# Performance work log

Measured on AMD Instinct MI355X. Metric: run time of the kernel, lower is better.

Reference implementation:

```python
import jax, jax.numpy as jnp
import numpy as np

N_NODES = 50000
N_EDGES = 800000
D_IN = 512
D_OUT = 128

def setup_inputs() -> dict:
    key = jax.random.key(0)
    k1, k2, k3, k4, k5, k6 = jax.random.split(key, 6)
    std = 1.0 / np.sqrt(D_OUT)
    x = jax.random.normal(k1, (N_NODES, D_IN), dtype=jnp.float32)
    edge_w = jax.random.uniform(k2, (N_EDGES,), dtype=jnp.float32)
    src = jax.random.randint(k3, (N_EDGES,), 0, N_NODES, dtype=jnp.int32)
    dst = jax.random.randint(k4, (N_EDGES,), 0, N_NODES, dtype=jnp.int32)
    W = jax.random.uniform(k5, (D_IN, D_OUT), minval=-std, maxval=std, dtype=jnp.float32)
    b = jax.random.uniform(k6, (D_OUT,), minval=-std, maxval=std, dtype=jnp.float32)
    return {"x": x, "edge_w": edge_w, "src": src, "dst": dst, "W": W, "b": b}

def reference(x, edge_w, src, dst, W, b):
    # Dense GEMM: [N, D_in] @ [D_in, D_out]
    h = x @ W
    # SpMM with COO adjacency: out[i] = sum_{e: dst[e]==i} edge_w[e] * h[src[e]]
    msg = h[src] * edge_w[:, None]          # [E, D_out]
    agg = jax.ops.segment_sum(msg, dst, num_segments=N_NODES)
    return agg + b
```

## Files before the change

kernel.cpp:

```cpp
#include <hip/hip_runtime.h>
#include <hip/hip_bf16.h>

#define M_NODES  50000
#define D_IN_K   512
#define D_OUT_N  128
#define N_EDGES  800000
#define SCAN_NBLK 49
#define PAD 16

typedef short  bf16x8 __attribute__((ext_vector_type(8)));
typedef float  f32x4  __attribute__((ext_vector_type(4)));

static __device__ __forceinline__ unsigned short f2bf(float f) {
    unsigned u = __float_as_uint(f);
    unsigned r = u + 0x7FFF + ((u >> 16) & 1);
    return (unsigned short)(r >> 16);
}
static __device__ __forceinline__ float bflo(unsigned q) { return __uint_as_float(q << 16); }
static __device__ __forceinline__ float bfhi(unsigned q) { return __uint_as_float(q & 0xFFFF0000u); }

__global__ __launch_bounds__(256) void permw_kernel(const float* __restrict__ W,
                                                    unsigned short* __restrict__ Wp) {
    int tid = blockIdx.x * 256 + threadIdx.x;
    int lane = tid & 63;
    int nt   = (tid >> 6) & 7;
    int kb4  = tid >> 9;
    int n    = nt * 16 + (lane & 15);
    int kbase = kb4 * 32 + ((lane >> 4) & 3) * 8;
    unsigned short frag[8];
#pragma unroll
    for (int j = 0; j < 8; ++j)
        frag[j] = f2bf(W[(size_t)(kbase + j) * D_OUT_N + n]);
    *(uint4*)&Wp[(size_t)tid * 8] = *(const uint4*)frag;
}

__global__ __launch_bounds__(256, 2) void mfma_gemm_hist_kernel(const float* __restrict__ x,
                                                                const uint4* __restrict__ Wp4,
                                                                unsigned short* __restrict__ h,
                                                                const int* __restrict__ dst,
                                                                int* __restrict__ counts) {
    __shared__ uint4 wlds[4096];

    const int wave = threadIdx.x >> 6;
    const int lane = threadIdx.x & 63;
    const int m0   = blockIdx.x * 128 + wave * 32;
    const int mrow = lane & 15;
    const int kgrp = lane >> 4;

    const int r0 = m0 + mrow;
    const int r1 = m0 + 16 + mrow;
    const float* xr0 = x + (size_t)((r0 < M_NODES) ? r0 : M_NODES - 1) * D_IN_K + kgrp * 8;
    const float* xr1 = x + (size_t)((r1 < M_NODES) ? r1 : M_NODES - 1) * D_IN_K + kgrp * 8;

    f32x4 acc[2][8];
#pragma unroll
    for (int f = 0; f < 2; ++f)
#pragma unroll
        for (int t = 0; t < 8; ++t) acc[f][t] = (f32x4){0.f, 0.f, 0.f, 0.f};

    for (int half = 0; half < 2; ++half) {
        __syncthreads();
#pragma unroll
        for (int i = 0; i < 16; ++i)
            wlds[threadIdx.x + i * 256] = Wp4[half * 4096 + threadIdx.x + i * 256];
        __syncthreads();

        const float* px0 = xr0 + half * 256;
        const float* px1 = xr1 + half * 256;

        float4 a00 = *(const float4*)(px0);
        float4 a01 = *(const float4*)(px0 + 4);
        float4 a10 = *(const float4*)(px1);
        float4 a11 = *(const float4*)(px1 + 4);

#pragma unroll
        for (int kb = 0; kb < 8; ++kb) {
            float4 n00, n01, n10, n11;
            if (kb < 7) {
                n00 = *(const float4*)(px0 + (kb + 1) * 32);
                n01 = *(const float4*)(px0 + (kb + 1) * 32 + 4);
                n10 = *(const float4*)(px1 + (kb + 1) * 32);
                n11 = *(const float4*)(px1 + (kb + 1) * 32 + 4);
            }

            union { bf16x8 v; __hip_bfloat162 h2[4]; } c0, c1;
            c0.h2[0] = __float22bfloat162_rn(make_float2(a00.x, a00.y));
            c0.h2[1] = __float22bfloat162_rn(make_float2(a00.z, a00.w));
            c0.h2[2] = __float22bfloat162_rn(make_float2(a01.x, a01.y));
            c0.h2[3] = __float22bfloat162_rn(make_float2(a01.z, a01.w));
            c1.h2[0] = __float22bfloat162_rn(make_float2(a10.x, a10.y));
            c1.h2[1] = __float22bfloat162_rn(make_float2(a10.z, a10.w));
            c1.h2[2] = __float22bfloat162_rn(make_float2(a11.x, a11.y));
            c1.h2[3] = __float22bfloat162_rn(make_float2(a11.z, a11.w));
            bf16x8 a0 = c0.v, a1 = c1.v;

#pragma unroll
            for (int nt = 0; nt < 8; ++nt) {
                union { uint4 u; bf16x8 v; } wb;
                wb.u = wlds[(kb * 8 + nt) * 64 + lane];
                acc[0][nt] = __builtin_amdgcn_mfma_f32_16x16x32_bf16(a0, wb.v, acc[0][nt], 0, 0, 0);
                acc[1][nt] = __builtin_amdgcn_mfma_f32_16x16x32_bf16(a1, wb.v, acc[1][nt], 0, 0, 0);
            }

            if (kb < 7) { a00 = n00; a01 = n01; a10 = n10; a11 = n11; }
        }
    }

#pragma unroll
    for (int f = 0; f < 2; ++f)
#pragma unroll
        for (int r = 0; r < 4; ++r) {
            int rr = m0 + f * 16 + kgrp * 4 + r;
            if (rr < M_NODES) {
                unsigned short* hp = h + (size_t)rr * D_OUT_N + mrow;
#pragma unroll
                for (int nt = 0; nt < 8; ++nt)
                    hp[nt * 16] = f2bf(acc[f][nt][r]);
            }
        }

    const int epb = (N_EDGES + gridDim.x - 1) / gridDim.x;
    const int e0  = blockIdx.x * epb;
    const int e1  = (e0 + epb < N_EDGES) ? e0 + epb : N_EDGES;
    for (int e = e0 + threadIdx.x; e < e1; e += 256)
        atomicAdd(&counts[dst[e] * PAD], 1);
}

__global__ __launch_bounds__(256) void scan_kernel(const int* __restrict__ counts,
                                                   int* __restrict__ offsets,
                                                   int* __restrict__ cursor,
                                                   int* __restrict__ partials,
                                                   int* __restrict__ flags) {
    __shared__ int wsum[4];
    __shared__ int carry_s;
    const int tid  = threadIdx.x;
    const int lane = tid & 63;
    const int wid  = tid >> 6;
    const int blk  = blockIdx.x;
    const int base = blk * 1024 + tid * 4;

    int v[4];
#pragma unroll
    for (int i = 0; i < 4; ++i)
        v[i] = (base + i < M_NODES) ? counts[(base + i) * PAD] : 0;
    int t = v[0] + v[1] + v[2] + v[3];

    int s = t;
#pragma unroll
    for (int d = 1; d < 64; d <<= 1) {
        int u = __shfl_up(s, d, 64);
        if (lane >= d) s += u;
    }
    if (lane == 63) wsum[wid] = s;
    __syncthreads();
    int wbase = 0;
#pragma unroll
    for (int w = 0; w < 4; ++w) wbase += (w < wid) ? wsum[w] : 0;
    int total = wsum[0] + wsum[1] + wsum[2] + wsum[3];

    if (tid == 0) {
        __hip_atomic_store(&partials[blk], total, __ATOMIC_RELAXED, __HIP_MEMORY_SCOPE_AGENT);
        __hip_atomic_store(&flags[blk], 1, __ATOMIC_RELEASE, __HIP_MEMORY_SCOPE_AGENT);
        if (blk == 0) offsets[M_NODES] = N_EDGES;
    }

    if (wid == 0) {
        int val = 0;
        if (lane < blk) {
            while (__hip_atomic_load(&flags[lane], __ATOMIC_ACQUIRE, __HIP_MEMORY_SCOPE_AGENT) == 0) {}
            val = __hip_atomic_load(&partials[lane], __ATOMIC_RELAXED, __HIP_MEMORY_SCOPE_AGENT);
        }
#pragma unroll
        for (int d = 32; d > 0; d >>= 1) val += __shfl_xor(val, d, 64);
        if (lane == 0) carry_s = val;
    }
    __syncthreads();
    const int carry = carry_s;

    int run = carry + wbase + s - t;
#pragma unroll
    for (int i = 0; i < 4; ++i) {
        if (base + i < M_NODES) {
            offsets[base + i] = run;
            cursor[(base + i) * PAD] = run;
        }
        run += v[i];
    }
}

__global__ __launch_bounds__(256) void fill_kernel(const int* __restrict__ src,
                                                   const int* __restrict__ dst,
                                                   const float* __restrict__ edge_w,
                                                   int* __restrict__ cursor,
                                                   int2* __restrict__ ep) {
    int e = blockIdx.x * blockDim.x + threadIdx.x;
    if (e >= N_EDGES) return;
    int d   = dst[e];
    int pos = atomicAdd(&cursor[d * PAD], 1);
    ep[pos] = make_int2(src[e], __float_as_int(edge_w[e]));
}

__global__ __launch_bounds__(256) void gather_kernel(const unsigned short* __restrict__ h,
                                                     const int2* __restrict__ ep,
                                                     const int* __restrict__ offsets,
                                                     const float* __restrict__ b,
                                                     float* __restrict__ out) {
    int t    = blockIdx.x * blockDim.x + threadIdx.x;
    int node = t >> 4;
    int lane = t & 15;
    if (node >= M_NODES) return;
    int beg = offsets[node];
    int end = offsets[node + 1];

    float4 b0 = *(const float4*)&b[lane * 8];
    float4 b1 = *(const float4*)&b[lane * 8 + 4];
    float a[4][8];
#pragma unroll
    for (int u = 0; u < 4; ++u)
#pragma unroll
        for (int c = 0; c < 8; ++c) a[u][c] = 0.f;

    int j = beg;
    for (; j + 4 <= end; j += 4) {
        int2 e0 = ep[j], e1 = ep[j + 1], e2 = ep[j + 2], e3 = ep[j + 3];
        uint4 q0 = *(const uint4*)(h + (size_t)e0.x * D_OUT_N + lane * 8);
        uint4 q1 = *(const uint4*)(h + (size_t)e1.x * D_OUT_N + lane * 8);
        uint4 q2 = *(const uint4*)(h + (size_t)e2.x * D_OUT_N + lane * 8);
        uint4 q3 = *(const uint4*)(h + (size_t)e3.x * D_OUT_N + lane * 8);
        float w0 = __int_as_float(e0.y), w1 = __int_as_float(e1.y);
        float w2 = __int_as_float(e2.y), w3 = __int_as_float(e3.y);
        a[0][0] += w0 * bflo(q0.x);  a[0][1] += w0 * bfhi(q0.x);
        a[0][2] += w0 * bflo(q0.y);  a[0][3] += w0 * bfhi(q0.y);
        a[0][4] += w0 * bflo(q0.z);  a[0][5] += w0 * bfhi(q0.z);
        a[0][6] += w0 * bflo(q0.w);  a[0][7] += w0 * bfhi(q0.w);
        a[1][0] += w1 * bflo(q1.x);  a[1][1] += w1 * bfhi(q1.x);
        a[1][2] += w1 * bflo(q1.y);  a[1][3] += w1 * bfhi(q1.y);
        a[1][4] += w1 * bflo(q1.z);  a[1][5] += w1 * bfhi(q1.z);
        a[1][6] += w1 * bflo(q1.w);  a[1][7] += w1 * bfhi(q1.w);
        a[2][0] += w2 * bflo(q2.x);  a[2][1] += w2 * bfhi(q2.x);
        a[2][2] += w2 * bflo(q2.y);  a[2][3] += w2 * bfhi(q2.y);
        a[2][4] += w2 * bflo(q2.z);  a[2][5] += w2 * bfhi(q2.z);
        a[2][6] += w2 * bflo(q2.w);  a[2][7] += w2 * bfhi(q2.w);
        a[3][0] += w3 * bflo(q3.x);  a[3][1] += w3 * bfhi(q3.x);
        a[3][2] += w3 * bflo(q3.y);  a[3][3] += w3 * bfhi(q3.y);
        a[3][4] += w3 * bflo(q3.z);  a[3][5] += w3 * bfhi(q3.z);
        a[3][6] += w3 * bflo(q3.w);  a[3][7] += w3 * bfhi(q3.w);
    }
    for (; j < end; ++j) {
        int2 e0 = ep[j];
        float w0 = __int_as_float(e0.y);
        uint4 q0 = *(const uint4*)(h + (size_t)e0.x * D_OUT_N + lane * 8);
        a[0][0] += w0 * bflo(q0.x);  a[0][1] += w0 * bfhi(q0.x);
        a[0][2] += w0 * bflo(q0.y);  a[0][3] += w0 * bfhi(q0.y);
        a[0][4] += w0 * bflo(q0.z);  a[0][5] += w0 * bfhi(q0.z);
        a[0][6] += w0 * bflo(q0.w);  a[0][7] += w0 * bfhi(q0.w);
    }

    float4 o0 = make_float4(b0.x + a[0][0] + a[1][0] + a[2][0] + a[3][0],
                            b0.y + a[0][1] + a[1][1] + a[2][1] + a[3][1],
                            b0.z + a[0][2] + a[1][2] + a[2][2] + a[3][2],
                            b0.w + a[0][3] + a[1][3] + a[2][3] + a[3][3]);
    float4 o1 = make_float4(b1.x + a[0][4] + a[1][4] + a[2][4] + a[3][4],
                            b1.y + a[0][5] + a[1][5] + a[2][5] + a[3][5],
                            b1.z + a[0][6] + a[1][6] + a[2][6] + a[3][6],
                            b1.w + a[0][7] + a[1][7] + a[2][7] + a[3][7]);
    float* op = &out[(size_t)node * D_OUT_N + lane * 8];
    *(float4*)op = o0;
    *(float4*)(op + 4) = o1;
}

extern "C" void kernel_launch(void* const* d_in, const int* in_sizes, int n_in,
                              void* d_out, int out_size, void* d_ws, size_t ws_size,
                              hipStream_t stream) {
    const float* x      = (const float*)d_in[0];
    const float* edge_w = (const float*)d_in[1];
    const int*   src    = (const int*)d_in[2];
    const int*   dst    = (const int*)d_in[3];
    const float* W      = (const float*)d_in[4];
    const float* b      = (const float*)d_in[5];
    float* out = (float*)d_out;

    char* wsp = (char*)d_ws;
    unsigned short* h = (unsigned short*)wsp;  wsp += (size_t)M_NODES * D_OUT_N * 2;
    int*   counts   = (int*)wsp;         wsp += (size_t)M_NODES * PAD * 4;
    int*   flags    = (int*)wsp;         wsp += 64 * 4;
    int*   cursor   = (int*)wsp;         wsp += (size_t)M_NODES * PAD * 4;
    int*   offsets  = (int*)wsp;         wsp += (((size_t)M_NODES + 1) * 4 + 15) & ~15ull;
    int2*  ep       = (int2*)wsp;        wsp += (size_t)N_EDGES * 8;
    unsigned short* Wp = (unsigned short*)wsp; wsp += (size_t)16 * 8 * 64 * 8 * 2;
    int*   partials = (int*)wsp;         wsp += (SCAN_NBLK * 4 + 15) & ~15ull;

    hipMemsetAsync(counts, 0, (size_t)M_NODES * PAD * 4 + 64 * 4, stream);
    permw_kernel<<<32, 256, 0, stream>>>(W, Wp);
    mfma_gemm_hist_kernel<<<(M_NODES + 127) / 128, 256, 0, stream>>>(
        x, (const uint4*)Wp, h, dst, counts);
    scan_kernel<<<SCAN_NBLK, 256, 0, stream>>>(counts, offsets, cursor, partials, flags);
    fill_kernel<<<(N_EDGES + 255) / 256, 256, 0, stream>>>(src, dst, edge_w, cursor, ep);
    gather_kernel<<<(int)(((long long)M_NODES * 16 + 255) / 256), 256, 0, stream>>>(
        h, ep, offsets, b, out);
}
```

Before: 290.4 us.

## Unpad counters, fold memset into permw, use direct LDS loads and vectorized fill

```diff
diff --git a/kernel.cpp b/kernel.cpp
--- a/kernel.cpp
+++ b/kernel.cpp
@@ -6,7 +6,6 @@
 #define D_OUT_N  128
 #define N_EDGES  800000
 #define SCAN_NBLK 49
-#define PAD 16
 
 typedef short  bf16x8 __attribute__((ext_vector_type(8)));
 typedef float  f32x4  __attribute__((ext_vector_type(4)));
@@ -19,8 +18,16 @@
 static __device__ __forceinline__ float bflo(unsigned q) { return __uint_as_float(q << 16); }
 static __device__ __forceinline__ float bfhi(unsigned q) { return __uint_as_float(q & 0xFFFF0000u); }
 
+static __device__ __forceinline__ void gl2lds16(const uint4* g, uint4* l) {
+    __builtin_amdgcn_global_load_lds(
+        (const __attribute__((address_space(1))) void*)g,
+        (__attribute__((address_space(3))) void*)l,
+        16, 0, 0);
+}
+
 __global__ __launch_bounds__(256) void permw_kernel(const float* __restrict__ W,
-                                                    unsigned short* __restrict__ Wp) {
+                                                    unsigned short* __restrict__ Wp,
+                                                    int* __restrict__ counts) {
     int tid = blockIdx.x * 256 + threadIdx.x;
     int lane = tid & 63;
     int nt   = (tid >> 6) & 7;
@@ -32,6 +39,8 @@
     for (int j = 0; j < 8; ++j)
         frag[j] = f2bf(W[(size_t)(kbase + j) * D_OUT_N + n]);
     *(uint4*)&Wp[(size_t)tid * 8] = *(const uint4*)frag;
+
+    for (int i = tid; i < M_NODES + 64; i += 8192) counts[i] = 0;
 }
 
 __global__ __launch_bounds__(256, 2) void mfma_gemm_hist_kernel(const float* __restrict__ x,
@@ -62,7 +71,8 @@
         __syncthreads();
 #pragma unroll
         for (int i = 0; i < 16; ++i)
-            wlds[threadIdx.x + i * 256] = Wp4[half * 4096 + threadIdx.x + i * 256];
+            gl2lds16(Wp4 + half * 4096 + threadIdx.x + i * 256,
+                     &wlds[threadIdx.x + i * 256]);
         __syncthreads();
 
         const float* px0 = xr0 + half * 256;
@@ -123,7 +133,7 @@
     const int e0  = blockIdx.x * epb;
     const int e1  = (e0 + epb < N_EDGES) ? e0 + epb : N_EDGES;
     for (int e = e0 + threadIdx.x; e < e1; e += 256)
-        atomicAdd(&counts[dst[e] * PAD], 1);
+        atomicAdd(&counts[dst[e]], 1);
 }
 
 __global__ __launch_bounds__(256) void scan_kernel(const int* __restrict__ counts,
@@ -140,9 +150,14 @@
     const int base = blk * 1024 + tid * 4;
 
     int v[4];
-#pragma unroll
-    for (int i = 0; i < 4; ++i)
-        v[i] = (base + i < M_NODES) ? counts[(base + i) * PAD] : 0;
+    if (base + 3 < M_NODES) {
+        int4 q = *(const int4*)&counts[base];
+        v[0] = q.x; v[1] = q.y; v[2] = q.z; v[3] = q.w;
+    } else {
+#pragma unroll
+        for (int i = 0; i < 4; ++i)
+            v[i] = (base + i < M_NODES) ? counts[base + i] : 0;
+    }
     int t = v[0] + v[1] + v[2] + v[3];
 
     int s = t;
@@ -182,7 +197,7 @@
     for (int i = 0; i < 4; ++i) {
         if (base + i < M_NODES) {
             offsets[base + i] = run;
-            cursor[(base + i) * PAD] = run;
+            cursor[base + i]  = run;
         }
         run += v[i];
     }
@@ -193,11 +208,19 @@
                                                    const float* __restrict__ edge_w,
                                                    int* __restrict__ cursor,
                                                    int2* __restrict__ ep) {
-    int e = blockIdx.x * blockDim.x + threadIdx.x;
-    if (e >= N_EDGES) return;
-    int d   = dst[e];
-    int pos = atomicAdd(&cursor[d * PAD], 1);
-    ep[pos] = make_int2(src[e], __float_as_int(edge_w[e]));
+    int base = (blockIdx.x * 256 + threadIdx.x) * 4;
+    if (base >= N_EDGES) return;
+    int4   s4 = *(const int4*)&src[base];
+    int4   d4 = *(const int4*)&dst[base];
+    float4 w4 = *(const float4*)&edge_w[base];
+    int p0 = atomicAdd(&cursor[d4.x], 1);
+    int p1 = atomicAdd(&cursor[d4.y], 1);
+    int p2 = atomicAdd(&cursor[d4.z], 1);
+    int p3 = atomicAdd(&cursor[d4.w], 1);
+    ep[p0] = make_int2(s4.x, __float_as_int(w4.x));
+    ep[p1] = make_int2(s4.y, __float_as_int(w4.y));
+    ep[p2] = make_int2(s4.z, __float_as_int(w4.z));
+    ep[p3] = make_int2(s4.w, __float_as_int(w4.w));
 }
 
 __global__ __launch_bounds__(256) void gather_kernel(const unsigned short* __restrict__ h,
@@ -282,20 +305,19 @@
 
     char* wsp = (char*)d_ws;
     unsigned short* h = (unsigned short*)wsp;  wsp += (size_t)M_NODES * D_OUT_N * 2;
-    int*   counts   = (int*)wsp;         wsp += (size_t)M_NODES * PAD * 4;
+    int*   counts   = (int*)wsp;         wsp += (size_t)M_NODES * 4;
     int*   flags    = (int*)wsp;         wsp += 64 * 4;
-    int*   cursor   = (int*)wsp;         wsp += (size_t)M_NODES * PAD * 4;
+    int*   cursor   = (int*)wsp;         wsp += (size_t)M_NODES * 4;
     int*   offsets  = (int*)wsp;         wsp += (((size_t)M_NODES + 1) * 4 + 15) & ~15ull;
     int2*  ep       = (int2*)wsp;        wsp += (size_t)N_EDGES * 8;
     unsigned short* Wp = (unsigned short*)wsp; wsp += (size_t)16 * 8 * 64 * 8 * 2;
     int*   partials = (int*)wsp;         wsp += (SCAN_NBLK * 4 + 15) & ~15ull;
 
-    hipMemsetAsync(counts, 0, (size_t)M_NODES * PAD * 4 + 64 * 4, stream);
-    permw_kernel<<<32, 256, 0, stream>>>(W, Wp);
+    permw_kernel<<<32, 256, 0, stream>>>(W, Wp, counts);
     mfma_gemm_hist_kernel<<<(M_NODES + 127) / 128, 256, 0, stream>>>(
         x, (const uint4*)Wp, h, dst, counts);
     scan_kernel<<<SCAN_NBLK, 256, 0, stream>>>(counts, offsets, cursor, partials, flags);
-    fill_kernel<<<(N_EDGES + 255) / 256, 256, 0, stream>>>(src, dst, edge_w, cursor, ep);
+    fill_kernel<<<(N_EDGES / 4 + 255) / 256, 256, 0, stream>>>(src, dst, edge_w, cursor, ep);
     gather_kernel<<<(int)(((long long)M_NODES * 16 + 255) / 256), 256, 0, stream>>>(
         h, ep, offsets, b, out);
 }
```

After: 289.4 us. About the same (-0.3%).
